# Kernel optimization log

Hardware: AMD Instinct MI355X
Metric: run time of the kernel (lower is better)

## Reference

```python
import jax, jax.numpy as jnp
import numpy as np
from jax.ops import segment_sum, segment_max

N = 50000        # nodes
E = 800000       # edges (before self loops)
IN_DIM = 128
HID = 16         # per-head out channels
HEADS = 4
NL = 3           # num GAT layers
OUT = 1
NG = 128         # number of graphs in the batch
NEG = 0.2        # LeakyReLU negative slope (PyG GATConv default)
EPS = 1e-5       # BatchNorm eps


def setup_inputs() -> dict:
    key = jax.random.key(0)
    ks = iter(jax.random.split(key, 64))
    inp = {}
    inp['x'] = jax.random.normal(next(ks), (N, IN_DIM), jnp.float32)
    inp['edge_index'] = jax.random.randint(next(ks), (2, E), 0, N, dtype=jnp.int32)
    inp['batch'] = jnp.sort(jax.random.randint(next(ks), (N,), 0, NG, dtype=jnp.int32))
    d = IN_DIM
    for l in range(NL):
        s = 1.0 / np.sqrt(d)
        inp[f'W{l}'] = jax.random.uniform(next(ks), (HEADS * HID, d), jnp.float32, -s, s)
        inp[f'att_src{l}'] = jax.random.normal(next(ks), (HEADS, HID), jnp.float32) * 0.1
        inp[f'att_dst{l}'] = jax.random.normal(next(ks), (HEADS, HID), jnp.float32) * 0.1
        inp[f'bias{l}'] = jnp.zeros((HEADS * HID,), jnp.float32)
        inp[f'gamma{l}'] = jnp.ones((HEADS * HID,), jnp.float32)
        inp[f'beta{l}'] = jnp.zeros((HEADS * HID,), jnp.float32)
        inp[f'mean{l}'] = jax.random.normal(next(ks), (HEADS * HID,), jnp.float32) * 0.1
        inp[f'var{l}'] = jax.random.uniform(next(ks), (HEADS * HID,), jnp.float32, 0.5, 1.5)
        d = HEADS * HID
    s = 1.0 / np.sqrt(d)
    inp['fcW'] = jax.random.uniform(next(ks), (OUT, d), jnp.float32, -s, s)
    inp['fcb'] = jnp.zeros((OUT,), jnp.float32)
    return inp


def gat_layer(x, src, dst, W, att_src, att_dst, bias):
    """PyG GATConv (concat=True). src/dst already include self loops."""
    n = x.shape[0]
    h = (x @ W.T).reshape(n, HEADS, HID)            # [N,H,C]
    a_s = jnp.sum(h * att_src, axis=-1)             # [N,H]
    a_d = jnp.sum(h * att_dst, axis=-1)             # [N,H]
    logits = a_s[src] + a_d[dst]                    # [Etot,H]
    logits = jnp.where(logits > 0, logits, NEG * logits)  # leaky_relu
    # scatter-softmax over destination-node neighborhoods
    m = segment_max(logits, dst, num_segments=n)
    e = jnp.exp(logits - m[dst])
    z = segment_sum(e, dst, num_segments=n)
    alpha = e / z[dst]                              # [Etot,H]
    out = segment_sum(h[src] * alpha[:, :, None], dst, num_segments=n)  # [N,H,C]
    return out.reshape(n, HEADS * HID) + bias, alpha


def reference(x, edge_index, batch,
              W0, att_src0, att_dst0, bias0, gamma0, beta0, mean0, var0,
              W1, att_src1, att_dst1, bias1, gamma1, beta1, mean1, var1,
              W2, att_src2, att_dst2, bias2, gamma2, beta2, mean2, var2,
              fcW, fcb):
    n = x.shape[0]
    loops = jnp.arange(n, dtype=edge_index.dtype)   # add_self_loops=True
    src = jnp.concatenate([edge_index[0], loops])
    dst = jnp.concatenate([edge_index[1], loops])
    params = [
        (W0, att_src0, att_dst0, bias0, gamma0, beta0, mean0, var0),
        (W1, att_src1, att_dst1, bias1, gamma1, beta1, mean1, var1),
        (W2, att_src2, att_dst2, bias2, gamma2, beta2, mean2, var2),
    ]
    h = x
    alpha0 = None
    for l, (W, a_s, a_d, b, g, be, mu, var) in enumerate(params):
        h, alpha = gat_layer(h, src, dst, W, a_s, a_d, b)
        if l == 0:
            alpha0 = alpha
        h = jax.nn.relu(h)
        h = g * (h - mu) / jnp.sqrt(var + EPS) + be  # BatchNorm1d (eval); dropout = identity
    # global_mean_pool over graph ids
    sums = segment_sum(h, batch, num_segments=NG)
    cnt = segment_sum(jnp.ones((n, 1), h.dtype), batch, num_segments=NG)
    pooled = sums / jnp.maximum(cnt, 1.0)
    out = jax.nn.sigmoid(pooled @ fcW.T + fcb)      # [NG, OUT]
    return out, alpha0
```

## Files before the change

kernel.cpp:

```cpp
#include <hip/hip_runtime.h>
#include <hip/hip_fp16.h>
#include <math.h>

#define NN     50000
#define EE     800000
#define ETOT   (EE + NN)
#define INDIM  128
#define HEADS  4
#define NG     128
#define NEGS   0.2f
#define BNEPS  1e-5f

typedef _Float16 half8 __attribute__((ext_vector_type(8)));
typedef _Float16 half4v __attribute__((ext_vector_type(4)));
typedef float floatx4 __attribute__((ext_vector_type(4)));


__global__ void degree_kernel(const int* __restrict__ ei, int* __restrict__ deg,
                              int* __restrict__ rank) {
    int e = blockIdx.x * blockDim.x + threadIdx.x;
    if (e >= ETOT) return;
    int d = (e < EE) ? ei[EE + e] : (e - EE);
    rank[e] = atomicAdd(&deg[d], 1);
}

__global__ void scan_block_kernel(const int* __restrict__ deg, int* __restrict__ rowstart,
                                  int* __restrict__ bsums) {
    __shared__ int tmp[1024];
    int tid = threadIdx.x;
    int i = blockIdx.x * 1024 + tid;
    int v = (i < NN) ? deg[i] : 0;
    tmp[tid] = v;
    __syncthreads();
    for (int off = 1; off < 1024; off <<= 1) {
        int t = (tid >= off) ? tmp[tid - off] : 0;
        __syncthreads();
        tmp[tid] += t;
        __syncthreads();
    }
    if (i < NN) rowstart[i] = tmp[tid] - v;
    if (tid == 1023) bsums[blockIdx.x] = tmp[tid];
}

__global__ void add_offsets_kernel(int* __restrict__ rowstart, const int* __restrict__ bsums) {
    int i = blockIdx.x * blockDim.x + threadIdx.x;
    if (i == 0) rowstart[NN] = ETOT;
    if (i >= NN) return;
    int nbk = i >> 10;
    int off = 0;
    for (int j = 0; j < nbk; ++j) off += bsums[j];
    rowstart[i] += off;
}

__global__ void scatter_kernel(const int* __restrict__ ei, const int* __restrict__ rowstart,
                               const int* __restrict__ rank, int* __restrict__ csr) {
    int e = blockIdx.x * blockDim.x + threadIdx.x;
    if (e >= ETOT) return;
    int s, d;
    if (e < EE) { s = ei[e]; d = ei[EE + e]; }
    else        { s = e - EE; d = e - EE; }
    int pos = rowstart[d] + rank[e];
    csr[pos] = s;
}

#define NX8 (NN * INDIM / 8)
#define PREP_TOT (NX8 + 2048 + NN + NG * 64 + NG)
__global__ __launch_bounds__(256) void prep_kernel(const float* __restrict__ x,
                                                   const float* __restrict__ W0,
                                                   const float* __restrict__ W1,
                                                   const float* __restrict__ W2,
                                                   _Float16* __restrict__ Xh,
                                                   _Float16* __restrict__ Wh,
                                                   int* __restrict__ deg,
                                                   float* __restrict__ psums,
                                                   int* __restrict__ pcnt) {
    int i = blockIdx.x * blockDim.x + threadIdx.x;
    if (i < NX8) {
        float4 v0 = *(const float4*)(x + (size_t)i * 8);
        float4 v1 = *(const float4*)(x + (size_t)i * 8 + 4);
        half8 o;
        o[0] = (_Float16)v0.x; o[1] = (_Float16)v0.y;
        o[2] = (_Float16)v0.z; o[3] = (_Float16)v0.w;
        o[4] = (_Float16)v1.x; o[5] = (_Float16)v1.y;
        o[6] = (_Float16)v1.z; o[7] = (_Float16)v1.w;
        *(half8*)(Xh + (size_t)i * 8) = o;
    } else if (i < NX8 + 2048) {
        int wi = (i - NX8) * 8;
#pragma unroll
        for (int j = 0; j < 8; ++j) {
            int idx = wi + j;
            float v = (idx < 8192) ? W0[idx]
                    : ((idx < 12288) ? W1[idx - 8192] : W2[idx - 12288]);
            Wh[idx] = (_Float16)v;
        }
    } else if (i < NX8 + 2048 + NN) {
        deg[i - NX8 - 2048] = 0;
    } else if (i < NX8 + 2048 + NN + NG * 64) {
        psums[i - NX8 - 2048 - NN] = 0.f;
    } else if (i < PREP_TOT) {
        pcnt[i - NX8 - 2048 - NN - NG * 64] = 0;
    }
}

template <int DD>
__global__ __launch_bounds__(256) void gemm_att_kernel(
    const _Float16* __restrict__ X, const _Float16* __restrict__ Wh,
    const float* __restrict__ attS, const float* __restrict__ attD,
    _Float16* __restrict__ H, float* __restrict__ AS, float* __restrict__ AD) {
    constexpr int KB = DD / 32;
    int tid = threadIdx.x;
    int wv = tid >> 6;
    int lane = tid & 63;
    int quad = lane >> 4;
    int n = lane & 15;
    int wbase = blockIdx.x * 64 + wv * 16;

    int arow = wbase + n;
    if (arow >= NN) arow = NN - 1;
    half8 a[KB];
#pragma unroll
    for (int kb = 0; kb < KB; ++kb)
        a[kb] = *(const half8*)(X + (size_t)arow * DD + kb * 32 + quad * 8);

    floatx4 c[4];
#pragma unroll
    for (int t = 0; t < 4; ++t) {
        floatx4 acc = {0.f, 0.f, 0.f, 0.f};
#pragma unroll
        for (int kb = 0; kb < KB; ++kb) {
            half8 b = *(const half8*)(Wh + (size_t)(t * 16 + n) * DD + kb * 32 + quad * 8);
            acc = __builtin_amdgcn_mfma_f32_16x16x32_f16(a[kb], b, acc, 0, 0, 0);
        }
        c[t] = acc;
    }

    float as_l[4], ad_l[4];
#pragma unroll
    for (int t = 0; t < 4; ++t) {
        as_l[t] = attS[t * 16 + n];
        ad_l[t] = attD[t * 16 + n];
    }
#pragma unroll
    for (int r = 0; r < 4; ++r) {
        int node = wbase + quad * 4 + r;
        bool ok = node < NN;
#pragma unroll
        for (int t = 0; t < 4; ++t) {
            float h = c[t][r];
            if (ok) H[(size_t)node * 64 + t * 16 + n] = (_Float16)h;
            float vs = h * as_l[t];
            float vd = h * ad_l[t];
#pragma unroll
            for (int off = 8; off; off >>= 1) {
                vs += __shfl_down(vs, off, 16);
                vd += __shfl_down(vd, off, 16);
            }
            if (ok && n == 0) {
                AS[node * 4 + t] = vs;
                AD[node * 4 + t] = vd;
            }
        }
    }
}

template <bool WRITE_Z>
__global__ __launch_bounds__(256) void edge_aggr_kernel(
    const _Float16* __restrict__ H, const float* __restrict__ AS,
    const float* __restrict__ AD,
    const int* __restrict__ rowstart,
    const int* __restrict__ csr,
    const float* __restrict__ bias, const float* __restrict__ gamma,
    const float* __restrict__ beta, const float* __restrict__ mean,
    const float* __restrict__ var, _Float16* __restrict__ Hout,
    float* __restrict__ Z) {
    int v = (blockIdx.x * blockDim.x + threadIdx.x) >> 6;
    if (v >= NN) return;
    int lane = threadIdx.x & 63;
    int q = lane >> 4;
    int l16 = lane & 15;
    int head = l16 >> 2;
    int ch4 = l16 * 4;
    float adv = AD[v * 4 + head];
    int start = rowstart[v];
    int cnt = rowstart[v + 1] - start;
    const int* srow = csr + start;
    float z = 0.f;
    float acc0 = 0.f, acc1 = 0.f, acc2 = 0.f, acc3 = 0.f;
    int k = 0;
    for (; k + 16 <= cnt; k += 16) {
        int b = k + q * 4;
        int s0 = srow[b + 0];
        int s1 = srow[b + 1];
        int s2 = srow[b + 2];
        int s3 = srow[b + 3];
        float a0 = AS[(size_t)s0 * 4 + head];
        float a1 = AS[(size_t)s1 * 4 + head];
        float a2 = AS[(size_t)s2 * 4 + head];
        float a3 = AS[(size_t)s3 * 4 + head];
        half4v h0 = *(const half4v*)(H + (size_t)s0 * 64 + ch4);
        half4v h1 = *(const half4v*)(H + (size_t)s1 * 64 + ch4);
        half4v h2 = *(const half4v*)(H + (size_t)s2 * 64 + ch4);
        half4v h3 = *(const half4v*)(H + (size_t)s3 * 64 + ch4);
        float l0 = a0 + adv; l0 = l0 > 0.f ? l0 : NEGS * l0; float p0 = __expf(l0);
        float l1 = a1 + adv; l1 = l1 > 0.f ? l1 : NEGS * l1; float p1 = __expf(l1);
        float l2 = a2 + adv; l2 = l2 > 0.f ? l2 : NEGS * l2; float p2 = __expf(l2);
        float l3 = a3 + adv; l3 = l3 > 0.f ? l3 : NEGS * l3; float p3 = __expf(l3);
        z += (p0 + p1) + (p2 + p3);
        acc0 = fmaf(p0, (float)h0[0], acc0); acc1 = fmaf(p0, (float)h0[1], acc1);
        acc2 = fmaf(p0, (float)h0[2], acc2); acc3 = fmaf(p0, (float)h0[3], acc3);
        acc0 = fmaf(p1, (float)h1[0], acc0); acc1 = fmaf(p1, (float)h1[1], acc1);
        acc2 = fmaf(p1, (float)h1[2], acc2); acc3 = fmaf(p1, (float)h1[3], acc3);
        acc0 = fmaf(p2, (float)h2[0], acc0); acc1 = fmaf(p2, (float)h2[1], acc1);
        acc2 = fmaf(p2, (float)h2[2], acc2); acc3 = fmaf(p2, (float)h2[3], acc3);
        acc0 = fmaf(p3, (float)h3[0], acc0); acc1 = fmaf(p3, (float)h3[1], acc1);
        acc2 = fmaf(p3, (float)h3[2], acc2); acc3 = fmaf(p3, (float)h3[3], acc3);
    }
    for (; k < cnt; k += 4) {
        int idx = k + q;
        if (idx < cnt) {
            int s = srow[idx];
            float a = AS[(size_t)s * 4 + head];
            half4v hv = *(const half4v*)(H + (size_t)s * 64 + ch4);
            float l = a + adv; l = l > 0.f ? l : NEGS * l;
            float p = __expf(l);
            z += p;
            acc0 = fmaf(p, (float)hv[0], acc0);
            acc1 = fmaf(p, (float)hv[1], acc1);
            acc2 = fmaf(p, (float)hv[2], acc2);
            acc3 = fmaf(p, (float)hv[3], acc3);
        }
    }
    z    += __shfl_xor(z, 16);    z    += __shfl_xor(z, 32);
    acc0 += __shfl_xor(acc0, 16); acc0 += __shfl_xor(acc0, 32);
    acc1 += __shfl_xor(acc1, 16); acc1 += __shfl_xor(acc1, 32);
    acc2 += __shfl_xor(acc2, 16); acc2 += __shfl_xor(acc2, 32);
    acc3 += __shfl_xor(acc3, 16); acc3 += __shfl_xor(acc3, 32);
    if (q == 0) {
        if (WRITE_Z && (l16 & 3) == 0) Z[v * 4 + head] = z;
        float4 bi = *(const float4*)(bias + ch4);
        float4 ga = *(const float4*)(gamma + ch4);
        float4 be = *(const float4*)(beta + ch4);
        float4 mu = *(const float4*)(mean + ch4);
        float4 va = *(const float4*)(var + ch4);
        float r0 = fmaxf(acc0 / z + bi.x, 0.f);
        float r1 = fmaxf(acc1 / z + bi.y, 0.f);
        float r2 = fmaxf(acc2 / z + bi.z, 0.f);
        float r3 = fmaxf(acc3 / z + bi.w, 0.f);
        r0 = ga.x * (r0 - mu.x) * rsqrtf(va.x + BNEPS) + be.x;
        r1 = ga.y * (r1 - mu.y) * rsqrtf(va.y + BNEPS) + be.y;
        r2 = ga.z * (r2 - mu.z) * rsqrtf(va.z + BNEPS) + be.z;
        r3 = ga.w * (r3 - mu.w) * rsqrtf(va.w + BNEPS) + be.w;
        half4v o;
        o[0] = (_Float16)r0;
        o[1] = (_Float16)r1;
        o[2] = (_Float16)r2;
        o[3] = (_Float16)r3;
        *(half4v*)(Hout + (size_t)v * 64 + ch4) = o;
    }
}

__global__ __launch_bounds__(256) void alpha_kernel(
    const int* __restrict__ ei,
    const float* __restrict__ AS, const float* __restrict__ AD,
    const float* __restrict__ Z, float* __restrict__ alpha_out) {
    int e = blockIdx.x * blockDim.x + threadIdx.x;
    if (e >= ETOT) return;
    int s, d;
    if (e < EE) { s = ei[e]; d = ei[EE + e]; }
    else        { s = e - EE; d = e - EE; }
    float4 as = *(const float4*)(AS + (size_t)s * 4);
    float4 ad = *(const float4*)(AD + (size_t)d * 4);
    float4 z4 = *(const float4*)(Z + (size_t)d * 4);
    float l;
    float4 a;
    l = as.x + ad.x; l = l > 0.f ? l : NEGS * l; a.x = __expf(l) / z4.x;
    l = as.y + ad.y; l = l > 0.f ? l : NEGS * l; a.y = __expf(l) / z4.y;
    l = as.z + ad.z; l = l > 0.f ? l : NEGS * l; a.z = __expf(l) / z4.z;
    l = as.w + ad.w; l = l > 0.f ? l : NEGS * l; a.w = __expf(l) / z4.w;
    *(float4*)(alpha_out + (size_t)e * 4) = a;
}

__global__ __launch_bounds__(256) void pool_kernel(const __half* __restrict__ H,
                                                   const int* __restrict__ batch,
                                                   float* __restrict__ sums,
                                                   int* __restrict__ cnt) {
    int wid = (blockIdx.x * blockDim.x + threadIdx.x) >> 6;
    int lane = threadIdx.x & 63;
    int base = wid * 64;
    if (base >= NN) return;
    int end = min(base + 64, NN);
    int cur = batch[base];
    float acc = 0.f;
    int c0 = 0;
    for (int i = base; i < end; ++i) {
        int g = batch[i];
        if (g != cur) {
            atomicAdd(&sums[cur * 64 + lane], acc);
            if (lane == 0) atomicAdd(&cnt[cur], c0);
            cur = g; acc = 0.f; c0 = 0;
        }
        acc += __half2float(H[(size_t)i * 64 + lane]);
        c0++;
    }
    atomicAdd(&sums[cur * 64 + lane], acc);
    if (lane == 0) atomicAdd(&cnt[cur], c0);
}

__global__ void fc_kernel(const float* __restrict__ sums, const int* __restrict__ cnt,
                          const float* __restrict__ fcW, const float* __restrict__ fcb,
                          float* __restrict__ out) {
    int g = (blockIdx.x * blockDim.x + threadIdx.x) >> 6;
    int lane = threadIdx.x & 63;
    if (g >= NG) return;
    float c = fmaxf((float)cnt[g], 1.f);
    float val = (sums[g * 64 + lane] / c) * fcW[lane];
#pragma unroll
    for (int off = 32; off; off >>= 1) val += __shfl_down(val, off, 64);
    if (lane == 0) out[g] = 1.f / (1.f + expf(-(val + fcb[0])));
}

extern "C" void kernel_launch(void* const* d_in, const int* in_sizes, int n_in,
                              void* d_out, int out_size, void* d_ws, size_t ws_size,
                              hipStream_t stream) {
    const float* x   = (const float*)d_in[0];
    const int* ei    = (const int*)d_in[1];
    const int* batch = (const int*)d_in[2];
    const float* W[3], *attS[3], *attD[3], *bias[3], *gamma[3], *beta[3], *mean[3], *var[3];
    for (int l = 0; l < 3; ++l) {
        W[l]     = (const float*)d_in[3 + 8 * l + 0];
        attS[l]  = (const float*)d_in[3 + 8 * l + 1];
        attD[l]  = (const float*)d_in[3 + 8 * l + 2];
        bias[l]  = (const float*)d_in[3 + 8 * l + 3];
        gamma[l] = (const float*)d_in[3 + 8 * l + 4];
        beta[l]  = (const float*)d_in[3 + 8 * l + 5];
        mean[l]  = (const float*)d_in[3 + 8 * l + 6];
        var[l]   = (const float*)d_in[3 + 8 * l + 7];
    }
    const float* fcW = (const float*)d_in[27];
    const float* fcb = (const float*)d_in[28];
    float* out = (float*)d_out;
    float* alpha_out = (float*)d_out + NG;

    char* p = (char*)d_ws;
    auto carve = [&](size_t bytes) {
        char* q = p;
        p += (bytes + 255) & ~(size_t)255;
        return q;
    };
    _Float16* Xh    = (_Float16*)carve(sizeof(_Float16) * NN * INDIM);
    _Float16* Wh    = (_Float16*)carve(sizeof(_Float16) * 16384);
    _Float16* Hh    = (_Float16*)carve(sizeof(_Float16) * NN * 64);
    _Float16* Hn    = (_Float16*)carve(sizeof(_Float16) * NN * 64);
    float* AS       = (float*)carve(sizeof(float) * NN * 4);
    float* AD       = (float*)carve(sizeof(float) * NN * 4);
    float* Z        = (float*)carve(sizeof(float) * NN * 4);
    int*   rowstart = (int*)carve(sizeof(int) * (NN + 1));
    int*   deg      = (int*)carve(sizeof(int) * NN);
    int*   rank     = (int*)carve(sizeof(int) * ETOT);
    int*   bsums    = (int*)carve(sizeof(int) * 64);
    int*   csr      = (int*)carve(sizeof(int) * ETOT);
    float* psums    = (float*)carve(sizeof(float) * NG * 64);
    int*   pcnt     = (int*)carve(sizeof(int) * NG);

    prep_kernel<<<(PREP_TOT + 255) / 256, 256, 0, stream>>>(
        x, W[0], W[1], W[2], Xh, Wh, deg, psums, pcnt);

    int nbScan = (NN + 1023) / 1024;
    degree_kernel<<<(ETOT + 255) / 256, 256, 0, stream>>>(ei, deg, rank);
    scan_block_kernel<<<nbScan, 1024, 0, stream>>>(deg, rowstart, bsums);
    add_offsets_kernel<<<(NN + 255) / 256, 256, 0, stream>>>(rowstart, bsums);
    scatter_kernel<<<(ETOT + 255) / 256, 256, 0, stream>>>(ei, rowstart, rank, csr);

    int edgeBlocks = (NN * 64 + 255) / 256;
    int posBlocks = (ETOT + 255) / 256;
    int gemmBlocks = (NN + 63) / 64;

    gemm_att_kernel<128><<<gemmBlocks, 256, 0, stream>>>(Xh, Wh, attS[0], attD[0],
                                                         Hh, AS, AD);
    edge_aggr_kernel<true><<<edgeBlocks, 256, 0, stream>>>(
        Hh, AS, AD, rowstart, csr,
        bias[0], gamma[0], beta[0], mean[0], var[0], Hn, Z);
    alpha_kernel<<<posBlocks, 256, 0, stream>>>(ei, AS, AD, Z, alpha_out);

    gemm_att_kernel<64><<<gemmBlocks, 256, 0, stream>>>(Hn, Wh + 8192, attS[1], attD[1],
                                                        Hh, AS, AD);
    edge_aggr_kernel<false><<<edgeBlocks, 256, 0, stream>>>(
        Hh, AS, AD, rowstart, csr,
        bias[1], gamma[1], beta[1], mean[1], var[1], Hn, nullptr);

    gemm_att_kernel<64><<<gemmBlocks, 256, 0, stream>>>(Hn, Wh + 12288, attS[2], attD[2],
                                                        Hh, AS, AD);
    edge_aggr_kernel<false><<<edgeBlocks, 256, 0, stream>>>(
        Hh, AS, AD, rowstart, csr,
        bias[2], gamma[2], beta[2], mean[2], var[2], Hn, nullptr);

    int poolWaves = (NN + 63) / 64;
    pool_kernel<<<(poolWaves * 64 + 255) / 256, 256, 0, stream>>>(
        (const __half*)Hn, batch, psums, pcnt);
    fc_kernel<<<(NG * 64 + 255) / 256, 256, 0, stream>>>(psums, pcnt, fcW, fcb, out);
}
```

Baseline: 364.7 us.

## Use wave-shuffle scan, interleave AD/Z, unify edge loop tail, shrink pool chunks

```diff
diff --git a/kernel.cpp b/kernel.cpp
--- a/kernel.cpp
+++ b/kernel.cpp
@@ -26,20 +26,34 @@
 
 __global__ void scan_block_kernel(const int* __restrict__ deg, int* __restrict__ rowstart,
                                   int* __restrict__ bsums) {
-    __shared__ int tmp[1024];
+    __shared__ int wsum[16];
     int tid = threadIdx.x;
+    int lane = tid & 63;
+    int w = tid >> 6;
     int i = blockIdx.x * 1024 + tid;
     int v = (i < NN) ? deg[i] : 0;
-    tmp[tid] = v;
+    int x = v;
+#pragma unroll
+    for (int off = 1; off < 64; off <<= 1) {
+        int t = __shfl_up(x, off, 64);
+        if (lane >= off) x += t;
+    }
+    if (lane == 63) wsum[w] = x;
     __syncthreads();
-    for (int off = 1; off < 1024; off <<= 1) {
-        int t = (tid >= off) ? tmp[tid - off] : 0;
-        __syncthreads();
-        tmp[tid] += t;
-        __syncthreads();
-    }
-    if (i < NN) rowstart[i] = tmp[tid] - v;
-    if (tid == 1023) bsums[blockIdx.x] = tmp[tid];
+    if (w == 0 && lane < 16) {
+        int s = wsum[lane];
+#pragma unroll
+        for (int off = 1; off < 16; off <<= 1) {
+            int t = __shfl_up(s, off, 16);
+            if ((lane & 15) >= off) s += t;
+        }
+        wsum[lane] = s;
+    }
+    __syncthreads();
+    int base = (w > 0) ? wsum[w - 1] : 0;
+    int incl = base + x;
+    if (i < NN) rowstart[i] = incl - v;
+    if (tid == 1023) bsums[blockIdx.x] = incl;
 }
 
 __global__ void add_offsets_kernel(int* __restrict__ rowstart, const int* __restrict__ bsums) {
@@ -106,7 +120,7 @@
 __global__ __launch_bounds__(256) void gemm_att_kernel(
     const _Float16* __restrict__ X, const _Float16* __restrict__ Wh,
     const float* __restrict__ attS, const float* __restrict__ attD,
-    _Float16* __restrict__ H, float* __restrict__ AS, float* __restrict__ AD) {
+    _Float16* __restrict__ H, float* __restrict__ AS, float* __restrict__ ADZ) {
     constexpr int KB = DD / 32;
     int tid = threadIdx.x;
     int wv = tid >> 6;
@@ -157,7 +171,7 @@
             }
             if (ok && n == 0) {
                 AS[node * 4 + t] = vs;
-                AD[node * 4 + t] = vd;
+                ADZ[(size_t)node * 8 + t] = vd;
             }
         }
     }
@@ -166,13 +180,12 @@
 template <bool WRITE_Z>
 __global__ __launch_bounds__(256) void edge_aggr_kernel(
     const _Float16* __restrict__ H, const float* __restrict__ AS,
-    const float* __restrict__ AD,
+    float* __restrict__ ADZ,
     const int* __restrict__ rowstart,
     const int* __restrict__ csr,
     const float* __restrict__ bias, const float* __restrict__ gamma,
     const float* __restrict__ beta, const float* __restrict__ mean,
-    const float* __restrict__ var, _Float16* __restrict__ Hout,
-    float* __restrict__ Z) {
+    const float* __restrict__ var, _Float16* __restrict__ Hout) {
     int v = (blockIdx.x * blockDim.x + threadIdx.x) >> 6;
     if (v >= NN) return;
     int lane = threadIdx.x & 63;
@@ -180,19 +193,19 @@
     int l16 = lane & 15;
     int head = l16 >> 2;
     int ch4 = l16 * 4;
-    float adv = AD[v * 4 + head];
+    float adv = ADZ[(size_t)v * 8 + head];
     int start = rowstart[v];
     int cnt = rowstart[v + 1] - start;
     const int* srow = csr + start;
+    int cm1 = cnt - 1;
     float z = 0.f;
     float acc0 = 0.f, acc1 = 0.f, acc2 = 0.f, acc3 = 0.f;
-    int k = 0;
-    for (; k + 16 <= cnt; k += 16) {
+    for (int k = 0; k < cnt; k += 16) {
         int b = k + q * 4;
-        int s0 = srow[b + 0];
-        int s1 = srow[b + 1];
-        int s2 = srow[b + 2];
-        int s3 = srow[b + 3];
+        int s0 = srow[min(b + 0, cm1)];
+        int s1 = srow[min(b + 1, cm1)];
+        int s2 = srow[min(b + 2, cm1)];
+        int s3 = srow[min(b + 3, cm1)];
         float a0 = AS[(size_t)s0 * 4 + head];
         float a1 = AS[(size_t)s1 * 4 + head];
         float a2 = AS[(size_t)s2 * 4 + head];
@@ -201,10 +214,14 @@
         half4v h1 = *(const half4v*)(H + (size_t)s1 * 64 + ch4);
         half4v h2 = *(const half4v*)(H + (size_t)s2 * 64 + ch4);
         half4v h3 = *(const half4v*)(H + (size_t)s3 * 64 + ch4);
-        float l0 = a0 + adv; l0 = l0 > 0.f ? l0 : NEGS * l0; float p0 = __expf(l0);
-        float l1 = a1 + adv; l1 = l1 > 0.f ? l1 : NEGS * l1; float p1 = __expf(l1);
-        float l2 = a2 + adv; l2 = l2 > 0.f ? l2 : NEGS * l2; float p2 = __expf(l2);
-        float l3 = a3 + adv; l3 = l3 > 0.f ? l3 : NEGS * l3; float p3 = __expf(l3);
+        float l0 = a0 + adv; l0 = l0 > 0.f ? l0 : NEGS * l0;
+        float l1 = a1 + adv; l1 = l1 > 0.f ? l1 : NEGS * l1;
+        float l2 = a2 + adv; l2 = l2 > 0.f ? l2 : NEGS * l2;
+        float l3 = a3 + adv; l3 = l3 > 0.f ? l3 : NEGS * l3;
+        float p0 = (b + 0 < cnt) ? __expf(l0) : 0.f;
+        float p1 = (b + 1 < cnt) ? __expf(l1) : 0.f;
+        float p2 = (b + 2 < cnt) ? __expf(l2) : 0.f;
+        float p3 = (b + 3 < cnt) ? __expf(l3) : 0.f;
         z += (p0 + p1) + (p2 + p3);
         acc0 = fmaf(p0, (float)h0[0], acc0); acc1 = fmaf(p0, (float)h0[1], acc1);
         acc2 = fmaf(p0, (float)h0[2], acc2); acc3 = fmaf(p0, (float)h0[3], acc3);
@@ -215,28 +232,13 @@
         acc0 = fmaf(p3, (float)h3[0], acc0); acc1 = fmaf(p3, (float)h3[1], acc1);
         acc2 = fmaf(p3, (float)h3[2], acc2); acc3 = fmaf(p3, (float)h3[3], acc3);
     }
-    for (; k < cnt; k += 4) {
-        int idx = k + q;
-        if (idx < cnt) {
-            int s = srow[idx];
-            float a = AS[(size_t)s * 4 + head];
-            half4v hv = *(const half4v*)(H + (size_t)s * 64 + ch4);
-            float l = a + adv; l = l > 0.f ? l : NEGS * l;
-            float p = __expf(l);
-            z += p;
-            acc0 = fmaf(p, (float)hv[0], acc0);
-            acc1 = fmaf(p, (float)hv[1], acc1);
-            acc2 = fmaf(p, (float)hv[2], acc2);
-            acc3 = fmaf(p, (float)hv[3], acc3);
-        }
-    }
     z    += __shfl_xor(z, 16);    z    += __shfl_xor(z, 32);
     acc0 += __shfl_xor(acc0, 16); acc0 += __shfl_xor(acc0, 32);
     acc1 += __shfl_xor(acc1, 16); acc1 += __shfl_xor(acc1, 32);
     acc2 += __shfl_xor(acc2, 16); acc2 += __shfl_xor(acc2, 32);
     acc3 += __shfl_xor(acc3, 16); acc3 += __shfl_xor(acc3, 32);
     if (q == 0) {
-        if (WRITE_Z && (l16 & 3) == 0) Z[v * 4 + head] = z;
+        if (WRITE_Z && (l16 & 3) == 0) ADZ[(size_t)v * 8 + 4 + head] = z;
         float4 bi = *(const float4*)(bias + ch4);
         float4 ga = *(const float4*)(gamma + ch4);
         float4 be = *(const float4*)(beta + ch4);
@@ -261,16 +263,17 @@
 
 __global__ __launch_bounds__(256) void alpha_kernel(
     const int* __restrict__ ei,
-    const float* __restrict__ AS, const float* __restrict__ AD,
-    const float* __restrict__ Z, float* __restrict__ alpha_out) {
+    const float* __restrict__ AS, const float* __restrict__ ADZ,
+    float* __restrict__ alpha_out) {
     int e = blockIdx.x * blockDim.x + threadIdx.x;
     if (e >= ETOT) return;
     int s, d;
     if (e < EE) { s = ei[e]; d = ei[EE + e]; }
     else        { s = e - EE; d = e - EE; }
     float4 as = *(const float4*)(AS + (size_t)s * 4);
-    float4 ad = *(const float4*)(AD + (size_t)d * 4);
-    float4 z4 = *(const float4*)(Z + (size_t)d * 4);
+    const float* row = ADZ + (size_t)d * 8;
+    float4 ad = *(const float4*)(row);
+    float4 z4 = *(const float4*)(row + 4);
     float l;
     float4 a;
     l = as.x + ad.x; l = l > 0.f ? l : NEGS * l; a.x = __expf(l) / z4.x;
@@ -286,9 +289,9 @@
                                                    int* __restrict__ cnt) {
     int wid = (blockIdx.x * blockDim.x + threadIdx.x) >> 6;
     int lane = threadIdx.x & 63;
-    int base = wid * 64;
+    int base = wid * 16;
     if (base >= NN) return;
-    int end = min(base + 64, NN);
+    int end = min(base + 16, NN);
     int cur = batch[base];
     float acc = 0.f;
     int c0 = 0;
@@ -352,8 +355,7 @@
     _Float16* Hh    = (_Float16*)carve(sizeof(_Float16) * NN * 64);
     _Float16* Hn    = (_Float16*)carve(sizeof(_Float16) * NN * 64);
     float* AS       = (float*)carve(sizeof(float) * NN * 4);
-    float* AD       = (float*)carve(sizeof(float) * NN * 4);
-    float* Z        = (float*)carve(sizeof(float) * NN * 4);
+    float* ADZ      = (float*)carve(sizeof(float) * NN * 8);
     int*   rowstart = (int*)carve(sizeof(int) * (NN + 1));
     int*   deg      = (int*)carve(sizeof(int) * NN);
     int*   rank     = (int*)carve(sizeof(int) * ETOT);
@@ -376,25 +378,25 @@
     int gemmBlocks = (NN + 63) / 64;
 
     gemm_att_kernel<128><<<gemmBlocks, 256, 0, stream>>>(Xh, Wh, attS[0], attD[0],
-                                                         Hh, AS, AD);
+                                                         Hh, AS, ADZ);
     edge_aggr_kernel<true><<<edgeBlocks, 256, 0, stream>>>(
-        Hh, AS, AD, rowstart, csr,
-        bias[0], gamma[0], beta[0], mean[0], var[0], Hn, Z);
-    alpha_kernel<<<posBlocks, 256, 0, stream>>>(ei, AS, AD, Z, alpha_out);
+        Hh, AS, ADZ, rowstart, csr,
+        bias[0], gamma[0], beta[0], mean[0], var[0], Hn);
+    alpha_kernel<<<posBlocks, 256, 0, stream>>>(ei, AS, ADZ, alpha_out);
 
     gemm_att_kernel<64><<<gemmBlocks, 256, 0, stream>>>(Hn, Wh + 8192, attS[1], attD[1],
-                                                        Hh, AS, AD);
+                                                        Hh, AS, ADZ);
     edge_aggr_kernel<false><<<edgeBlocks, 256, 0, stream>>>(
-        Hh, AS, AD, rowstart, csr,
-        bias[1], gamma[1], beta[1], mean[1], var[1], Hn, nullptr);
+        Hh, AS, ADZ, rowstart, csr,
+        bias[1], gamma[1], beta[1], mean[1], var[1], Hn);
 
     gemm_att_kernel<64><<<gemmBlocks, 256, 0, stream>>>(Hn, Wh + 12288, attS[2], attD[2],
-                                                        Hh, AS, AD);
+                                                        Hh, AS, ADZ);
     edge_aggr_kernel<false><<<edgeBlocks, 256, 0, stream>>>(
-        Hh, AS, AD, rowstart, csr,
-        bias[2], gamma[2], beta[2], mean[2], var[2], Hn, nullptr);
-
-    int poolWaves = (NN + 63) / 64;
+        Hh, AS, ADZ, rowstart, csr,
+        bias[2], gamma[2], beta[2], mean[2], var[2], Hn);
+
+    int poolWaves = (NN + 15) / 16;
     pool_kernel<<<(poolWaves * 64 + 255) / 256, 256, 0, stream>>>(
         (const __half*)Hn, batch, psums, pcnt);
     fc_kernel<<<(NG * 64 + 255) / 256, 256, 0, stream>>>(psums, pcnt, fcW, fcb, out);
```

New measurement: 346.8 us. 4.9% less time.
